# Performance work log

Measured on AMD Instinct MI355X. Metric: run time of the kernel, lower is better.

Reference implementation:

```python
import jax, jax.numpy as jnp
import numpy as np

N = 100000      # nodes
E = 300000      # directed edges (avg degree ~3, ogbn-arxiv-like sparsity)
F_IN = 128      # ogbn-arxiv node features
H = 256         # hidden
C = 40          # ogbn-arxiv classes
L = 6           # num_layers
BN_EPS = 1e-5


def setup_inputs() -> dict:
    key = jax.random.key(0)
    ks = jax.random.split(key, 12)
    x = jax.random.normal(ks[0], (N, F_IN), jnp.float32)
    edge_index = jax.random.randint(ks[1], (2, E), 0, N, dtype=jnp.int32)
    s_in = 1.0 / np.sqrt(F_IN)
    s_h = 1.0 / np.sqrt(H)
    return {
        "x": x,
        "edge_index": edge_index,
        "w_in": jax.random.normal(ks[2], (F_IN, H), jnp.float32) * s_in,
        "b_in": jnp.zeros((H,), jnp.float32),
        "conv_w": jax.random.normal(ks[3], (L, H, H), jnp.float32) * s_h,
        "conv_b": jnp.zeros((L, H), jnp.float32),
        "bn_gamma": jnp.ones((L, H), jnp.float32),
        "bn_beta": jnp.zeros((L, H), jnp.float32),
        "out_w": jax.random.normal(ks[4], (H, C), jnp.float32) * s_h,
        "out_b": jnp.zeros((C,), jnp.float32),
        "res_weights": jax.random.normal(ks[5], (L,), jnp.float32),
    }


def _gcn_norm(edge_index, n_nodes):
    # GCNConv default: add self-loops, symmetric normalization D^-1/2 (A+I) D^-1/2
    loops = jnp.arange(n_nodes, dtype=edge_index.dtype)
    src = jnp.concatenate([edge_index[0], loops])
    dst = jnp.concatenate([edge_index[1], loops])
    deg = jax.ops.segment_sum(jnp.ones_like(dst, jnp.float32), dst, num_segments=n_nodes)
    dinv = jax.lax.rsqrt(jnp.maximum(deg, 1.0))
    norm = dinv[src] * dinv[dst]  # [E+N]
    return src, dst, norm


def _batchnorm(h, gamma, beta):
    # BatchNorm1d in training mode: biased batch statistics over nodes
    m = jnp.mean(h, axis=0)
    v = jnp.mean(jnp.square(h - m), axis=0)
    return (h - m) * jax.lax.rsqrt(v + BN_EPS) * gamma + beta


def reference(x, edge_index, w_in, b_in, conv_w, conv_b, bn_gamma, bn_beta, out_w, out_b, res_weights):
    src, dst, norm = _gcn_norm(edge_index, N)
    h = x @ w_in + b_in            # input_fc: [N, H]
    x_input = h
    layer_out = []
    prev = None
    for i in range(L):
        hw = h @ conv_w[i]                                  # linear transform
        msg = hw[src] * norm[:, None]                       # gather + scale
        agg = jax.ops.segment_sum(msg, dst, num_segments=N) + conv_b[i]  # scatter-add
        a = jax.nn.relu(_batchnorm(agg, bn_gamma[i], bn_beta[i]))
        # dropout p=0.5 omitted (eval mode / deterministic reference)
        if i == 0:
            h = a + 0.2 * x_input
        else:
            h = a + 0.2 * x_input + 0.7 * prev
        layer_out.append(h)
        prev = h
    w = jax.nn.softmax(res_weights)                          # [L]
    mix = jnp.einsum('lnh,l->nh', jnp.stack(layer_out), w)   # weighted sum of layer outputs
    logits = mix @ out_w + out_b                             # [N, C]
    return jax.nn.log_softmax(logits, axis=1)
```

## Files before the change

kernel.cpp:

```cpp
#include <hip/hip_runtime.h>
#include <math.h>

#define Nn   100000
#define Ee   300000
#define FIN  128
#define Hdim 256
#define Ncls 40
#define Lnum 6
#define SCAN_B 98

typedef __attribute__((ext_vector_type(8))) short bf16x8;
typedef __attribute__((ext_vector_type(4))) float f32x4;

__device__ __forceinline__ float bf2f(unsigned int u16) {
    unsigned int x = u16 << 16;
    return __builtin_bit_cast(float, x);
}
__device__ __forceinline__ unsigned short f2bf(float f) {
    unsigned int x = __builtin_bit_cast(unsigned int, f);
    x = (x + 0x7FFFu + ((x >> 16) & 1u)) >> 16;
    return (unsigned short)x;
}
__device__ __forceinline__ void unpack2(unsigned int u, float& lo, float& hi) {
    lo = __builtin_bit_cast(float, u << 16);
    hi = __builtin_bit_cast(float, u & 0xFFFF0000u);
}
__device__ __forceinline__ unsigned int pack2(float a, float b) {
    return (unsigned int)f2bf(a) | ((unsigned int)f2bf(b) << 16);
}

__global__ void count_edges(const int* __restrict__ ei, int* __restrict__ cnt) {
    int e = blockIdx.x * blockDim.x + threadIdx.x;
    if (e < Ee) atomicAdd(&cnt[ei[Ee + e]], 1);
}

__global__ void scan_block(const int* __restrict__ cnt, int* __restrict__ iscan,
                           int* __restrict__ btot) {
    __shared__ int buf[1024];
    int t = threadIdx.x;
    int g = blockIdx.x * 1024 + t;
    int v = (g < Nn) ? cnt[g] : 0;
    buf[t] = v; __syncthreads();
    for (int off = 1; off < 1024; off <<= 1) {
        int x = buf[t];
        int a = (t >= off) ? buf[t - off] : 0;
        __syncthreads();
        buf[t] = x + a;
        __syncthreads();
    }
    if (g < Nn) iscan[g] = buf[t];
    if (t == 1023) btot[blockIdx.x] = buf[1023];
}

__global__ void scan_tops(const int* __restrict__ btot, int* __restrict__ bpref) {
    __shared__ int b[128];
    int t = threadIdx.x;
    int v = (t < SCAN_B) ? btot[t] : 0;
    b[t] = v; __syncthreads();
    for (int off = 1; off < 128; off <<= 1) {
        int x = b[t];
        int a = (t >= off) ? b[t - off] : 0;
        __syncthreads();
        b[t] = x + a;
        __syncthreads();
    }
    if (t < SCAN_B) bpref[t] = b[t] - v;
}

__global__ void scan_final(const int* __restrict__ cnt, const int* __restrict__ iscan,
                           const int* __restrict__ bpref, int* __restrict__ offs,
                           float* __restrict__ dinvp) {
    int g = blockIdx.x * 1024 + threadIdx.x;
    if (g < Nn) {
        int c = cnt[g];
        offs[g] = bpref[blockIdx.x] + iscan[g] - c;
        dinvp[g] = rsqrtf((float)(c + 1));
    }
    if (g == 0) offs[Nn] = Ee;
}

__global__ void fill_csr(const int* __restrict__ ei, const int* __restrict__ offs,
                         int* __restrict__ cur, const float* __restrict__ dinvp,
                         int* __restrict__ esrc, float* __restrict__ ew) {
    int e = blockIdx.x * blockDim.x + threadIdx.x;
    if (e >= Ee) return;
    int s = ei[e], d = ei[Ee + e];
    int p = offs[d] + atomicAdd(&cur[d], 1);
    esrc[p] = s;
    ew[p] = dinvp[s];
}

__global__ void prep_weights(const float* __restrict__ conv_w, const float* __restrict__ w_in,
                             const float* __restrict__ out_w,
                             unsigned short* __restrict__ Whi,
                             unsigned short* __restrict__ Fhi,
                             unsigned short* __restrict__ Whd, unsigned short* __restrict__ Wld) {
    int b = blockIdx.x, t = threadIdx.x;
    if (b < 1536) {
        int id = b * 256 + t;
        int l = id >> 16, k = (id >> 8) & 255, n = id & 255;
        Whi[l * 65536 + n * 256 + k] = f2bf(conv_w[id]);
    } else if (b < 1664) {
        int id = (b - 1536) * 256 + t;
        int k = id >> 8, n = id & 255;
        Fhi[n * FIN + k] = f2bf(w_in[id]);
    } else {
        int id = (b - 1664) * 256 + t;
        int c = id >> 8, k = id & 255;
        float w = (c < Ncls) ? out_w[k * Ncls + c] : 0.f;
        unsigned short hi = f2bf(w);
        unsigned short lo = f2bf(w - bf2f(hi));
        Whd[c * 256 + k] = hi;
        Wld[c * 256 + k] = lo;
    }
}

__global__ void cvt_bf16(const float* __restrict__ src, unsigned short* __restrict__ dst, int n8) {
    int i = blockIdx.x * blockDim.x + threadIdx.x;
    if (i >= n8) return;
    float4 a = ((const float4*)src)[i * 2];
    float4 b = ((const float4*)src)[i * 2 + 1];
    uint4 o;
    o.x = pack2(a.x, a.y); o.y = pack2(a.z, a.w);
    o.z = pack2(b.x, b.y); o.w = pack2(b.z, b.w);
    ((uint4*)dst)[i] = o;
}

__global__ void agg_kernel(const unsigned short* __restrict__ Hin,
                           unsigned short* __restrict__ T,
                           const int* __restrict__ offs, const int* __restrict__ esrc,
                           const float* __restrict__ ew, const float* __restrict__ dinvp,
                           float* __restrict__ bnsum, float* __restrict__ bnsq) {
    int t = threadIdx.x;
    if (blockIdx.x == 0) { bnsum[t] = 0.f; bnsq[t] = 0.f; }
    int wv = t >> 6, lane = t & 63;
    int n = blockIdx.x * 4 + wv;
    int o0 = offs[n], o1 = offs[n + 1];
    float dn = dinvp[n];
    uint2 u = *(const uint2*)&Hin[(size_t)n * Hdim + lane * 4];
    float a0, a1, a2, a3;
    unpack2(u.x, a0, a1); unpack2(u.y, a2, a3);
    a0 *= dn; a1 *= dn; a2 *= dn; a3 *= dn;
    for (int e = o0; e < o1; ++e) {
        int s = esrc[e];
        float w = ew[e];
        uint2 us = *(const uint2*)&Hin[(size_t)s * Hdim + lane * 4];
        float v0, v1, v2, v3;
        unpack2(us.x, v0, v1); unpack2(us.y, v2, v3);
        a0 += w * v0; a1 += w * v1; a2 += w * v2; a3 += w * v3;
    }
    uint2 o;
    o.x = pack2(dn * a0, dn * a1); o.y = pack2(dn * a2, dn * a3);
    *(uint2*)&T[(size_t)n * Hdim + lane * 4] = o;
}

__global__ __launch_bounds__(512) void gemm_mfma(
    const unsigned short* __restrict__ A, unsigned short* __restrict__ C,
    const unsigned short* __restrict__ W,
    const float* __restrict__ bias, int K, int nrows,
    float* __restrict__ bnsum, float* __restrict__ bnsq, int do_stats)
{
    __shared__ __align__(16) unsigned short smem[18432];
    __shared__ float lsum[256];
    __shared__ float lsq[256];

    const int t    = threadIdx.x;
    const int lane = t & 63, wid = t >> 6;
    const int ln   = lane & 15, quad = lane >> 4;
    const int r64  = (wid >> 2) * 64, c64 = (wid & 3) * 64;
    const int r0   = blockIdx.x * 128;

    if (t < 256) { lsum[t] = 0.f; lsq[t] = 0.f; }

    unsigned short* At = smem;
    unsigned short* Bt = smem + 5120;

    f32x4 acc[4][4];
#pragma unroll
    for (int i = 0; i < 4; ++i)
#pragma unroll
        for (int j = 0; j < 4; ++j) acc[i][j] = (f32x4){0.f, 0.f, 0.f, 0.f};

    const int arow = t >> 2, akq = t & 3;
    const bool arow_ok = (r0 + arow < nrows);
    const int nk = K >> 5;

    uint4 ga = make_uint4(0u, 0u, 0u, 0u);
    if (arow_ok) ga = *(const uint4*)&A[(size_t)(r0 + arow) * K + akq * 8];
    uint4 gb[2];
#pragma unroll
    for (int q = 0; q < 2; ++q) {
        int idx = t + 512 * q, row = idx >> 2, kq = idx & 3;
        gb[q] = *(const uint4*)&W[(size_t)row * K + kq * 8];
    }

    for (int kt = 0; kt < nk; ++kt) {
        __syncthreads();
        *(uint4*)&At[arow * 40 + akq * 8] = ga;
#pragma unroll
        for (int q = 0; q < 2; ++q) {
            int idx = t + 512 * q, row = idx >> 2, kq = idx & 3;
            *(uint4*)&Bt[row * 40 + kq * 8] = gb[q];
        }
        __syncthreads();
        if (kt + 1 < nk) {
            int k0 = (kt + 1) << 5;
            ga = make_uint4(0u, 0u, 0u, 0u);
            if (arow_ok) ga = *(const uint4*)&A[(size_t)(r0 + arow) * K + k0 + akq * 8];
#pragma unroll
            for (int q = 0; q < 2; ++q) {
                int idx = t + 512 * q, row = idx >> 2, kq = idx & 3;
                gb[q] = *(const uint4*)&W[(size_t)row * K + k0 + kq * 8];
            }
        }
        bf16x8 af[4], bf[4];
#pragma unroll
        for (int rt = 0; rt < 4; ++rt)
            af[rt] = *(const bf16x8*)&At[(r64 + rt * 16 + ln) * 40 + quad * 8];
#pragma unroll
        for (int ct = 0; ct < 4; ++ct)
            bf[ct] = *(const bf16x8*)&Bt[(c64 + ct * 16 + ln) * 40 + quad * 8];
#pragma unroll
        for (int rt = 0; rt < 4; ++rt)
#pragma unroll
            for (int ct = 0; ct < 4; ++ct)
                acc[rt][ct] = __builtin_amdgcn_mfma_f32_16x16x32_bf16(af[rt], bf[ct], acc[rt][ct], 0, 0, 0);
    }
    __syncthreads();

    float bc[4];
#pragma unroll
    for (int ct = 0; ct < 4; ++ct) bc[ct] = bias[c64 + ct * 16 + ln];

    if (do_stats) {
#pragma unroll
        for (int ct = 0; ct < 4; ++ct) {
            float s = 0.f, qq = 0.f;
#pragma unroll
            for (int rt = 0; rt < 4; ++rt)
#pragma unroll
                for (int v = 0; v < 4; ++v) {
                    int row = r0 + r64 + rt * 16 + quad * 4 + v;
                    if (row < nrows) {
                        float val = acc[rt][ct][v] + bc[ct];
                        s += val; qq += val * val;
                    }
                }
            s  += __shfl_xor(s, 16);  s  += __shfl_xor(s, 32);
            qq += __shfl_xor(qq, 16); qq += __shfl_xor(qq, 32);
            if (quad == 0) { atomicAdd(&lsum[c64 + ct * 16 + ln], s); atomicAdd(&lsq[c64 + ct * 16 + ln], qq); }
        }
    }

    unsigned short* Tt = &smem[wid * 2304];
    const int rr2 = lane & 31, jh = lane >> 5;
#pragma unroll
    for (int h = 0; h < 2; ++h) {
#pragma unroll
        for (int rr = 0; rr < 2; ++rr) {
            int rt = 2 * h + rr;
#pragma unroll
            for (int ct = 0; ct < 4; ++ct)
#pragma unroll
                for (int v = 0; v < 4; ++v)
                    Tt[(rr * 16 + quad * 4 + v) * 72 + ct * 16 + ln] = f2bf(acc[rt][ct][v] + bc[ct]);
        }
        __asm__ volatile("s_waitcnt lgkmcnt(0)" ::: "memory");
        int grow = r0 + r64 + h * 32 + rr2;
        if (grow < nrows) {
#pragma unroll
            for (int j = 0; j < 4; ++j) {
                uint4 v4 = *(const uint4*)&Tt[rr2 * 72 + jh * 32 + j * 8];
                *(uint4*)&C[(size_t)grow * 256 + c64 + jh * 32 + j * 8] = v4;
            }
        }
        __asm__ volatile("s_waitcnt lgkmcnt(0)" ::: "memory");
    }

    if (do_stats) {
        __syncthreads();
        if (t < 256) { atomicAdd(&bnsum[t], lsum[t]); atomicAdd(&bnsq[t], lsq[t]); }
    }
}

__global__ void apply_kernel(const unsigned short* __restrict__ T,
                             const unsigned short* __restrict__ X,
                             unsigned short* __restrict__ Hb, unsigned short* __restrict__ M,
                             const float* __restrict__ bnsum, const float* __restrict__ bnsq,
                             const float* __restrict__ gamma, const float* __restrict__ beta,
                             const float* __restrict__ res_w, int layer) {
    __shared__ float sc[256], sh[256];
    int t = threadIdx.x;
    {
        float mean = bnsum[t] * (1.0f / Nn);
        float var  = fmaxf(bnsq[t] * (1.0f / Nn) - mean * mean, 0.f);
        float rstd = rsqrtf(var + 1e-5f);
        float s = gamma[t] * rstd;
        sc[t] = s; sh[t] = beta[t] - mean * s;
    }
    float m0 = res_w[0];
#pragma unroll
    for (int i = 1; i < Lnum; ++i) m0 = fmaxf(m0, res_w[i]);
    float se = 0.f, wl = 0.f;
#pragma unroll
    for (int i = 0; i < Lnum; ++i) {
        float e = __expf(res_w[i] - m0);
        se += e;
        if (i == layer) wl = e;
    }
    float wi = wl / se;
    __syncthreads();

    int idx = blockIdx.x * blockDim.x + t;
    int c8 = idx & 31;
    float scl[8], shl[8];
#pragma unroll
    for (int k = 0; k < 8; ++k) { scl[k] = sc[c8 * 8 + k]; shl[k] = sh[c8 * 8 + k]; }

    uint4 tv = ((const uint4*)T)[idx];
    uint4 xv = ((const uint4*)X)[idx];
    float tf[8], xf[8];
    unpack2(tv.x, tf[0], tf[1]); unpack2(tv.y, tf[2], tf[3]);
    unpack2(tv.z, tf[4], tf[5]); unpack2(tv.w, tf[6], tf[7]);
    unpack2(xv.x, xf[0], xf[1]); unpack2(xv.y, xf[2], xf[3]);
    unpack2(xv.z, xf[4], xf[5]); unpack2(xv.w, xf[6], xf[7]);

    float a[8];
#pragma unroll
    for (int k = 0; k < 8; ++k)
        a[k] = fmaxf(tf[k] * scl[k] + shl[k], 0.f) + 0.2f * xf[k];
    if (layer > 0) {
        uint4 hv = ((const uint4*)Hb)[idx];
        float hf[8];
        unpack2(hv.x, hf[0], hf[1]); unpack2(hv.y, hf[2], hf[3]);
        unpack2(hv.z, hf[4], hf[5]); unpack2(hv.w, hf[6], hf[7]);
#pragma unroll
        for (int k = 0; k < 8; ++k) a[k] += 0.7f * hf[k];
    }
    uint4 ho;
    ho.x = pack2(a[0], a[1]); ho.y = pack2(a[2], a[3]);
    ho.z = pack2(a[4], a[5]); ho.w = pack2(a[6], a[7]);
    ((uint4*)Hb)[idx] = ho;

    float m[8];
    if (layer == 0) {
#pragma unroll
        for (int k = 0; k < 8; ++k) m[k] = wi * a[k];
    } else {
        uint4 mv = ((const uint4*)M)[idx];
        float mf[8];
        unpack2(mv.x, mf[0], mf[1]); unpack2(mv.y, mf[2], mf[3]);
        unpack2(mv.z, mf[4], mf[5]); unpack2(mv.w, mf[6], mf[7]);
#pragma unroll
        for (int k = 0; k < 8; ++k) m[k] = mf[k] + wi * a[k];
    }
    uint4 mo;
    mo.x = pack2(m[0], m[1]); mo.y = pack2(m[2], m[3]);
    mo.z = pack2(m[4], m[5]); mo.w = pack2(m[6], m[7]);
    ((uint4*)M)[idx] = mo;
}

__global__ __launch_bounds__(512) void head_mfma(const unsigned short* __restrict__ M,
                                                 const unsigned short* __restrict__ Whd,
                                                 const unsigned short* __restrict__ Wld,
                                                 const float* __restrict__ out_b,
                                                 float* __restrict__ out, int nrows) {
    __shared__ unsigned short At[128 * 40];
    const int t    = threadIdx.x;
    const int lane = t & 63, wid = t >> 6;
    const int ln   = lane & 15, quad = lane >> 4;
    const int r0   = blockIdx.x * 128;

    f32x4 acc[3];
#pragma unroll
    for (int ct = 0; ct < 3; ++ct) acc[ct] = (f32x4){0.f, 0.f, 0.f, 0.f};

    for (int k0 = 0; k0 < 256; k0 += 32) {
        __syncthreads();
        {
            int row = t >> 2, kq = t & 3;
            uint4 g = make_uint4(0u, 0u, 0u, 0u);
            if (r0 + row < nrows)
                g = *(const uint4*)&M[(size_t)(r0 + row) * 256 + k0 + kq * 8];
            *(uint4*)&At[row * 40 + kq * 8] = g;
        }
        __syncthreads();
        bf16x8 af = *(const bf16x8*)&At[(wid * 16 + ln) * 40 + quad * 8];
#pragma unroll
        for (int ct = 0; ct < 3; ++ct) {
            int c = ct * 16 + ln;
            bf16x8 bh = *(const bf16x8*)&Whd[c * 256 + k0 + quad * 8];
            bf16x8 bl = *(const bf16x8*)&Wld[c * 256 + k0 + quad * 8];
            acc[ct] = __builtin_amdgcn_mfma_f32_16x16x32_bf16(af, bh, acc[ct], 0, 0, 0);
            acc[ct] = __builtin_amdgcn_mfma_f32_16x16x32_bf16(af, bl, acc[ct], 0, 0, 0);
        }
    }

    int   cc[3]; float bias[3];
#pragma unroll
    for (int ct = 0; ct < 3; ++ct) {
        cc[ct] = ct * 16 + ln;
        bias[ct] = (cc[ct] < Ncls) ? out_b[cc[ct]] : 0.f;
    }
#pragma unroll
    for (int v = 0; v < 4; ++v) {
        int row = r0 + wid * 16 + quad * 4 + v;
        float val[3];
#pragma unroll
        for (int ct = 0; ct < 3; ++ct) val[ct] = acc[ct][v] + bias[ct];
        float mx = -1e30f;
#pragma unroll
        for (int ct = 0; ct < 3; ++ct) if (cc[ct] < Ncls) mx = fmaxf(mx, val[ct]);
        mx = fmaxf(mx, __shfl_xor(mx, 1)); mx = fmaxf(mx, __shfl_xor(mx, 2));
        mx = fmaxf(mx, __shfl_xor(mx, 4)); mx = fmaxf(mx, __shfl_xor(mx, 8));
        float s = 0.f;
#pragma unroll
        for (int ct = 0; ct < 3; ++ct) if (cc[ct] < Ncls) s += __expf(val[ct] - mx);
        s += __shfl_xor(s, 1); s += __shfl_xor(s, 2);
        s += __shfl_xor(s, 4); s += __shfl_xor(s, 8);
        float lse = mx + __logf(s);
        if (row < nrows) {
            out[(size_t)row * Ncls + cc[0]] = val[0] - lse;
            out[(size_t)row * Ncls + cc[1]] = val[1] - lse;
            if (ln < 8) out[(size_t)row * Ncls + cc[2]] = val[2] - lse;
        }
    }
}

extern "C" void kernel_launch(void* const* d_in, const int* in_sizes, int n_in,
                              void* d_out, int out_size, void* d_ws, size_t ws_size,
                              hipStream_t stream)
{
    const float* x      = (const float*)d_in[0];
    const int*   ei     = (const int*)d_in[1];
    const float* w_in   = (const float*)d_in[2];
    const float* b_in   = (const float*)d_in[3];
    const float* conv_w = (const float*)d_in[4];
    const float* conv_b = (const float*)d_in[5];
    const float* gamma  = (const float*)d_in[6];
    const float* beta   = (const float*)d_in[7];
    const float* out_w  = (const float*)d_in[8];
    const float* out_b  = (const float*)d_in[9];
    const float* res_w  = (const float*)d_in[10];
    float* out = (float*)d_out;
    char* ws = (char*)d_ws;

    int*   cnt    = (int*)  (ws + 0);
    int*   cursor = (int*)  (ws + 400000);
    int*   offs   = (int*)  (ws + 800000);
    float* dinvp  = (float*)(ws + 1200016);
    int*   esrc   = (int*)  (ws + 1600016);
    float* ew     = (float*)(ws + 2800016);
    float* bnsum  = (float*)(ws + 4000016);
    float* bnsq   = (float*)(ws + 4001040);
    int*   iscan  = (int*)  (ws + 4002064);
    int*   btot   = (int*)  (ws + 4402064);
    int*   bpref  = (int*)  (ws + 4402576);
    unsigned short* Whi = (unsigned short*)(ws + 4403088);
    unsigned short* Fhi = (unsigned short*)(ws + 5975952);
    unsigned short* Whd = (unsigned short*)(ws + 6107024);
    unsigned short* Wld = (unsigned short*)(ws + 6131600);
    unsigned short* X   = (unsigned short*)(ws + 6156176);
    unsigned short* Hb  = X  + (size_t)Nn * Hdim;
    unsigned short* T   = Hb + (size_t)Nn * Hdim;
    unsigned short* M   = T  + (size_t)Nn * Hdim;
    unsigned short* xbf = M;

    hipMemsetAsync(cnt, 0, 800000, stream);

    count_edges<<<(Ee + 255) / 256, 256, 0, stream>>>(ei, cnt);
    scan_block<<<SCAN_B, 1024, 0, stream>>>(cnt, iscan, btot);
    scan_tops<<<1, 128, 0, stream>>>(btot, bpref);
    scan_final<<<SCAN_B, 1024, 0, stream>>>(cnt, iscan, bpref, offs, dinvp);
    fill_csr<<<(Ee + 255) / 256, 256, 0, stream>>>(ei, offs, cursor, dinvp, esrc, ew);

    prep_weights<<<1712, 256, 0, stream>>>(conv_w, w_in, out_w,
                                           Whi, Fhi, Whd, Wld);
    cvt_bf16<<<(Nn * FIN / 8 + 255) / 256, 256, 0, stream>>>(x, xbf, Nn * FIN / 8);

    const int gblocks = (Nn + 127) / 128;
    gemm_mfma<<<gblocks, 512, 0, stream>>>(xbf, X, Fhi, b_in, FIN, Nn,
                                           nullptr, nullptr, 0);

    for (int i = 0; i < Lnum; ++i) {
        agg_kernel<<<Nn / 4, 256, 0, stream>>>(i == 0 ? X : Hb, T, offs, esrc, ew, dinvp,
                                               bnsum, bnsq);
        gemm_mfma<<<gblocks, 512, 0, stream>>>(T, T,
                                               Whi + (size_t)i * Hdim * Hdim,
                                               conv_b + (size_t)i * Hdim,
                                               Hdim, Nn, bnsum, bnsq, 1);
        apply_kernel<<<(Nn * 32) / 256, 256, 0, stream>>>(T, X, Hb, M,
                                                          bnsum, bnsq,
                                                          gamma + (size_t)i * Hdim,
                                                          beta + (size_t)i * Hdim,
                                                          res_w, i);
    }

    head_mfma<<<gblocks, 512, 0, stream>>>(M, Whd, Wld, out_b, out, Nn);
}
```

Baseline: 1.271 ms.

## Fuse neighbor aggregation into GEMM A-tile staging and drop agg kernel

The separate sparse aggregation kernel is removed. The CSR gather and normalization are now done inside the GEMM's A-tile prefetch: each thread accumulates its row's neighbor contributions for the current 32-wide K slice before staging it to shared memory. This avoids writing and re-reading the aggregated intermediate and saves one launch per layer. BatchNorm statistics get per-layer buffers that are zeroed by the initial memset. In exchange, the edge list is walked once per K tile, and gather latency now sits inside the GEMM pipeline.

```diff
diff --git a/kernel.cpp b/kernel.cpp
--- a/kernel.cpp
+++ b/kernel.cpp
@@ -126,38 +126,13 @@
     ((uint4*)dst)[i] = o;
 }
 
-__global__ void agg_kernel(const unsigned short* __restrict__ Hin,
-                           unsigned short* __restrict__ T,
-                           const int* __restrict__ offs, const int* __restrict__ esrc,
-                           const float* __restrict__ ew, const float* __restrict__ dinvp,
-                           float* __restrict__ bnsum, float* __restrict__ bnsq) {
-    int t = threadIdx.x;
-    if (blockIdx.x == 0) { bnsum[t] = 0.f; bnsq[t] = 0.f; }
-    int wv = t >> 6, lane = t & 63;
-    int n = blockIdx.x * 4 + wv;
-    int o0 = offs[n], o1 = offs[n + 1];
-    float dn = dinvp[n];
-    uint2 u = *(const uint2*)&Hin[(size_t)n * Hdim + lane * 4];
-    float a0, a1, a2, a3;
-    unpack2(u.x, a0, a1); unpack2(u.y, a2, a3);
-    a0 *= dn; a1 *= dn; a2 *= dn; a3 *= dn;
-    for (int e = o0; e < o1; ++e) {
-        int s = esrc[e];
-        float w = ew[e];
-        uint2 us = *(const uint2*)&Hin[(size_t)s * Hdim + lane * 4];
-        float v0, v1, v2, v3;
-        unpack2(us.x, v0, v1); unpack2(us.y, v2, v3);
-        a0 += w * v0; a1 += w * v1; a2 += w * v2; a3 += w * v3;
-    }
-    uint2 o;
-    o.x = pack2(dn * a0, dn * a1); o.y = pack2(dn * a2, dn * a3);
-    *(uint2*)&T[(size_t)n * Hdim + lane * 4] = o;
-}
-
+template <int FUSED>
 __global__ __launch_bounds__(512) void gemm_mfma(
     const unsigned short* __restrict__ A, unsigned short* __restrict__ C,
     const unsigned short* __restrict__ W,
     const float* __restrict__ bias, int K, int nrows,
+    const int* __restrict__ offs, const int* __restrict__ esrc,
+    const float* __restrict__ ew, const float* __restrict__ dinvp,
     float* __restrict__ bnsum, float* __restrict__ bnsq, int do_stats)
 {
     __shared__ __align__(16) unsigned short smem[18432];
@@ -182,11 +157,43 @@
         for (int j = 0; j < 4; ++j) acc[i][j] = (f32x4){0.f, 0.f, 0.f, 0.f};
 
     const int arow = t >> 2, akq = t & 3;
-    const bool arow_ok = (r0 + arow < nrows);
+    const int nsrow = r0 + arow;
+    const bool arow_ok = (nsrow < nrows);
     const int nk = K >> 5;
 
-    uint4 ga = make_uint4(0u, 0u, 0u, 0u);
-    if (arow_ok) ga = *(const uint4*)&A[(size_t)(r0 + arow) * K + akq * 8];
+    int eo0 = 0, eo1 = 0; float dn = 0.f;
+    if (FUSED && arow_ok) { eo0 = offs[nsrow]; eo1 = offs[nsrow + 1]; dn = dinvp[nsrow]; }
+
+    auto stage_a = [&](int k0) -> uint4 {
+        if (!FUSED) {
+            uint4 g = make_uint4(0u, 0u, 0u, 0u);
+            if (arow_ok) g = *(const uint4*)&A[(size_t)nsrow * K + k0 + akq * 8];
+            return g;
+        }
+        if (!arow_ok) return make_uint4(0u, 0u, 0u, 0u);
+        uint4 h = *(const uint4*)&A[(size_t)nsrow * 256 + k0 + akq * 8];
+        float f[8];
+        unpack2(h.x, f[0], f[1]); unpack2(h.y, f[2], f[3]);
+        unpack2(h.z, f[4], f[5]); unpack2(h.w, f[6], f[7]);
+#pragma unroll
+        for (int j = 0; j < 8; ++j) f[j] *= dn;
+        for (int e = eo0; e < eo1; ++e) {
+            int s = esrc[e];
+            float w = ew[e];
+            uint4 hs = *(const uint4*)&A[(size_t)s * 256 + k0 + akq * 8];
+            float g[8];
+            unpack2(hs.x, g[0], g[1]); unpack2(hs.y, g[2], g[3]);
+            unpack2(hs.z, g[4], g[5]); unpack2(hs.w, g[6], g[7]);
+#pragma unroll
+            for (int j = 0; j < 8; ++j) f[j] = fmaf(w, g[j], f[j]);
+        }
+        uint4 o;
+        o.x = pack2(dn * f[0], dn * f[1]); o.y = pack2(dn * f[2], dn * f[3]);
+        o.z = pack2(dn * f[4], dn * f[5]); o.w = pack2(dn * f[6], dn * f[7]);
+        return o;
+    };
+
+    uint4 ga = stage_a(0);
     uint4 gb[2];
 #pragma unroll
     for (int q = 0; q < 2; ++q) {
@@ -205,26 +212,25 @@
         __syncthreads();
         if (kt + 1 < nk) {
             int k0 = (kt + 1) << 5;
-            ga = make_uint4(0u, 0u, 0u, 0u);
-            if (arow_ok) ga = *(const uint4*)&A[(size_t)(r0 + arow) * K + k0 + akq * 8];
+            ga = stage_a(k0);
 #pragma unroll
             for (int q = 0; q < 2; ++q) {
                 int idx = t + 512 * q, row = idx >> 2, kq = idx & 3;
                 gb[q] = *(const uint4*)&W[(size_t)row * K + k0 + kq * 8];
             }
         }
-        bf16x8 af[4], bf[4];
+        bf16x8 af[4], bfr[4];
 #pragma unroll
         for (int rt = 0; rt < 4; ++rt)
             af[rt] = *(const bf16x8*)&At[(r64 + rt * 16 + ln) * 40 + quad * 8];
 #pragma unroll
         for (int ct = 0; ct < 4; ++ct)
-            bf[ct] = *(const bf16x8*)&Bt[(c64 + ct * 16 + ln) * 40 + quad * 8];
+            bfr[ct] = *(const bf16x8*)&Bt[(c64 + ct * 16 + ln) * 40 + quad * 8];
 #pragma unroll
         for (int rt = 0; rt < 4; ++rt)
 #pragma unroll
             for (int ct = 0; ct < 4; ++ct)
-                acc[rt][ct] = __builtin_amdgcn_mfma_f32_16x16x32_bf16(af[rt], bf[ct], acc[rt][ct], 0, 0, 0);
+                acc[rt][ct] = __builtin_amdgcn_mfma_f32_16x16x32_bf16(af[rt], bfr[ct], acc[rt][ct], 0, 0, 0);
     }
     __syncthreads();
 
@@ -267,12 +273,13 @@
         }
         __asm__ volatile("s_waitcnt lgkmcnt(0)" ::: "memory");
         int grow = r0 + r64 + h * 32 + rr2;
+        uint4 v4[4];
+#pragma unroll
+        for (int j = 0; j < 4; ++j) v4[j] = *(const uint4*)&Tt[rr2 * 72 + jh * 32 + j * 8];
         if (grow < nrows) {
 #pragma unroll
-            for (int j = 0; j < 4; ++j) {
-                uint4 v4 = *(const uint4*)&Tt[rr2 * 72 + jh * 32 + j * 8];
-                *(uint4*)&C[(size_t)grow * 256 + c64 + jh * 32 + j * 8] = v4;
-            }
+            for (int j = 0; j < 4; ++j)
+                *(uint4*)&C[(size_t)grow * 256 + c64 + jh * 32 + j * 8] = v4[j];
         }
         __asm__ volatile("s_waitcnt lgkmcnt(0)" ::: "memory");
     }
@@ -447,26 +454,25 @@
 
     int*   cnt    = (int*)  (ws + 0);
     int*   cursor = (int*)  (ws + 400000);
-    int*   offs   = (int*)  (ws + 800000);
-    float* dinvp  = (float*)(ws + 1200016);
-    int*   esrc   = (int*)  (ws + 1600016);
-    float* ew     = (float*)(ws + 2800016);
-    float* bnsum  = (float*)(ws + 4000016);
-    float* bnsq   = (float*)(ws + 4001040);
-    int*   iscan  = (int*)  (ws + 4002064);
-    int*   btot   = (int*)  (ws + 4402064);
-    int*   bpref  = (int*)  (ws + 4402576);
-    unsigned short* Whi = (unsigned short*)(ws + 4403088);
-    unsigned short* Fhi = (unsigned short*)(ws + 5975952);
-    unsigned short* Whd = (unsigned short*)(ws + 6107024);
-    unsigned short* Wld = (unsigned short*)(ws + 6131600);
-    unsigned short* X   = (unsigned short*)(ws + 6156176);
+    float* bnstat = (float*)(ws + 800000);
+    int*   offs   = (int*)  (ws + 812288);
+    float* dinvp  = (float*)(ws + 1212304);
+    int*   esrc   = (int*)  (ws + 1612304);
+    float* ew     = (float*)(ws + 2812304);
+    int*   iscan  = (int*)  (ws + 4012304);
+    int*   btot   = (int*)  (ws + 4412304);
+    int*   bpref  = (int*)  (ws + 4412816);
+    unsigned short* Whi = (unsigned short*)(ws + 4413328);
+    unsigned short* Fhi = (unsigned short*)(ws + 5199760);
+    unsigned short* Whd = (unsigned short*)(ws + 5265296);
+    unsigned short* Wld = (unsigned short*)(ws + 5289872);
+    unsigned short* X   = (unsigned short*)(ws + 5314560);
     unsigned short* Hb  = X  + (size_t)Nn * Hdim;
     unsigned short* T   = Hb + (size_t)Nn * Hdim;
     unsigned short* M   = T  + (size_t)Nn * Hdim;
     unsigned short* xbf = M;
 
-    hipMemsetAsync(cnt, 0, 800000, stream);
+    hipMemsetAsync(cnt, 0, 812288, stream);
 
     count_edges<<<(Ee + 255) / 256, 256, 0, stream>>>(ei, cnt);
     scan_block<<<SCAN_B, 1024, 0, stream>>>(cnt, iscan, btot);
@@ -479,18 +485,21 @@
     cvt_bf16<<<(Nn * FIN / 8 + 255) / 256, 256, 0, stream>>>(x, xbf, Nn * FIN / 8);
 
     const int gblocks = (Nn + 127) / 128;
-    gemm_mfma<<<gblocks, 512, 0, stream>>>(xbf, X, Fhi, b_in, FIN, Nn,
-                                           nullptr, nullptr, 0);
+    gemm_mfma<0><<<gblocks, 512, 0, stream>>>(xbf, X, Fhi, b_in, FIN, Nn,
+                                              nullptr, nullptr, nullptr, nullptr,
+                                              nullptr, nullptr, 0);
 
     for (int i = 0; i < Lnum; ++i) {
-        agg_kernel<<<Nn / 4, 256, 0, stream>>>(i == 0 ? X : Hb, T, offs, esrc, ew, dinvp,
-                                               bnsum, bnsq);
-        gemm_mfma<<<gblocks, 512, 0, stream>>>(T, T,
-                                               Whi + (size_t)i * Hdim * Hdim,
-                                               conv_b + (size_t)i * Hdim,
-                                               Hdim, Nn, bnsum, bnsq, 1);
+        float* bsum = bnstat + i * 512;
+        float* bsq  = bsum + 256;
+        gemm_mfma<1><<<gblocks, 512, 0, stream>>>(i == 0 ? X : Hb, T,
+                                                  Whi + (size_t)i * Hdim * Hdim,
+                                                  conv_b + (size_t)i * Hdim,
+                                                  Hdim, Nn,
+                                                  offs, esrc, ew, dinvp,
+                                                  bsum, bsq, 1);
         apply_kernel<<<(Nn * 32) / 256, 256, 0, stream>>>(T, X, Hb, M,
-                                                          bnsum, bnsq,
+                                                          bsum, bsq,
                                                           gamma + (size_t)i * Hdim,
                                                           beta + (size_t)i * Hdim,
                                                           res_w, i);
```

Result: slower. 1.337 ms (+5.2%).
